# Optimization experiments

Hardware: AMD Instinct MI355X
Metric: run time of the kernel (lower is better)

Reference implementation:

```python
import jax, jax.numpy as jnp
import numpy as np

B, N, C, K, H = 64, 4096, 256, 8, 256  # H = max(dim, hidden_dim=128)
ITERS = 3
EPS = 1e-8


def _ln(x, g, b):
    # torch LayerNorm: biased variance, eps=1e-5
    m = x.mean(-1, keepdims=True)
    v = ((x - m) ** 2).mean(-1, keepdims=True)
    return (x - m) * jax.lax.rsqrt(v + 1e-5) * g + b


def setup_inputs() -> dict:
    key = jax.random.key(0)
    ks = jax.random.split(key, 16)
    s = 0.02
    d = {}
    d['inputs'] = jax.random.normal(ks[0], (B, N, C), jnp.float32)
    d['slots_noise'] = jax.random.normal(ks[1], (K, C), jnp.float32)  # eval-mode shared noise
    d['mu'] = jax.random.normal(ks[2], (C,), jnp.float32)
    d['log_sigma'] = jax.random.normal(ks[3], (C,), jnp.float32) * 0.1
    d['ln_in_g'] = jnp.ones((C,), jnp.float32); d['ln_in_b'] = jnp.zeros((C,), jnp.float32)
    d['ln_s_g'] = jnp.ones((C,), jnp.float32); d['ln_s_b'] = jnp.zeros((C,), jnp.float32)
    d['ln_ff_g'] = jnp.ones((C,), jnp.float32); d['ln_ff_b'] = jnp.zeros((C,), jnp.float32)
    d['Wq'] = jax.random.normal(ks[4], (C, C), jnp.float32) * s; d['bq'] = jnp.zeros((C,), jnp.float32)
    d['Wk'] = jax.random.normal(ks[5], (C, C), jnp.float32) * s; d['bk'] = jnp.zeros((C,), jnp.float32)
    d['Wv'] = jax.random.normal(ks[6], (C, C), jnp.float32) * s; d['bv'] = jnp.zeros((C,), jnp.float32)
    d['W_ih'] = jax.random.normal(ks[7], (C, 3 * C), jnp.float32) * s; d['b_ih'] = jnp.zeros((3 * C,), jnp.float32)
    d['W_hh'] = jax.random.normal(ks[8], (C, 3 * C), jnp.float32) * s; d['b_hh'] = jnp.zeros((3 * C,), jnp.float32)
    d['W1'] = jax.random.normal(ks[9], (C, H), jnp.float32) * s; d['b1'] = jnp.zeros((H,), jnp.float32)
    d['W2'] = jax.random.normal(ks[10], (H, C), jnp.float32) * s; d['b2'] = jnp.zeros((C,), jnp.float32)
    return d


def reference(inputs, slots_noise, mu, log_sigma,
              ln_in_g, ln_in_b, ln_s_g, ln_s_b, ln_ff_g, ln_ff_b,
              Wq, bq, Wk, bk, Wv, bv,
              W_ih, b_ih, W_hh, b_hh,
              W1, b1, W2, b2):
    scale = C ** (-0.5)
    # eval-mode slot init: mu + exp(log_sigma) * noise, shared across batch
    slots = jnp.broadcast_to(mu + jnp.exp(log_sigma) * slots_noise, (B, K, C))
    x = _ln(inputs, ln_in_g, ln_in_b)
    k = x @ Wk + bk  # [B,N,C]
    v = x @ Wv + bv  # [B,N,C]
    for _ in range(ITERS):
        slots_prev = slots
        sn = _ln(slots, ln_s_g, ln_s_b)
        q = sn @ Wq + bq  # [B,K,C]
        dots = jnp.einsum('bid,bjd->bij', q, k) * scale  # [B,K,N]
        attn = jax.nn.softmax(dots, axis=1) + EPS  # softmax over slots (queries)
        attn = attn / attn.sum(-1, keepdims=True)  # renormalize over keys
        updates = jnp.einsum('bjd,bij->bid', v, attn)  # [B,K,C]
        # torch GRUCell
        gx = updates @ W_ih + b_ih
        gh = slots_prev @ W_hh + b_hh
        xr, xz, xn = jnp.split(gx, 3, axis=-1)
        hr, hz, hn = jnp.split(gh, 3, axis=-1)
        r = jax.nn.sigmoid(xr + hr)
        z = jax.nn.sigmoid(xz + hz)
        n = jnp.tanh(xn + r * hn)
        slots = (1.0 - z) * n + z * slots_prev
        pre = _ln(slots, ln_ff_g, ln_ff_b)
        slots = slots + (jax.nn.relu(pre @ W1 + b1) @ W2 + b2)
    return slots
```

## Files before the change

kernel.cpp:

```cpp
#include <hip/hip_runtime.h>
#include <hip/hip_bf16.h>

#define B_ 64
#define N_ 4096
#define C_ 256
#define K_ 8
#define M_ (B_*N_)
#define ITERS_ 3
#define SCALE_ 0.0625f
#define EPS_ 1e-8f

typedef __attribute__((ext_vector_type(4))) float f32x4;
typedef __attribute__((ext_vector_type(8))) __bf16 bf16x8;
typedef __attribute__((ext_vector_type(8))) unsigned short ushort8;
typedef __attribute__((ext_vector_type(4))) unsigned short ushort4v;

static __device__ __forceinline__ unsigned short f2bf(float f){
    union { float f; unsigned u; } v; v.f = f;
    unsigned r = v.u + 0x7fffu + ((v.u >> 16) & 1u);
    return (unsigned short)(r >> 16);
}
static __device__ __forceinline__ float bf2f(unsigned short h){
    union { unsigned u; float f; } v; v.u = ((unsigned)h) << 16;
    return v.f;
}

__global__ void prep1_kernel(const float* __restrict__ mu, const float* __restrict__ lsig,
                             const float* __restrict__ noise, float* __restrict__ slots){
    int idx = blockIdx.x*256 + threadIdx.x;
    int c = idx & 255, i = (idx >> 8) & 7;
    slots[idx] = mu[c] + expf(lsig[c])*noise[i*256 + c];
}

__global__ void prep2_kernel(const float* __restrict__ Wq, const float* __restrict__ Wk,
                             const float* __restrict__ bq, const float* __restrict__ bk,
                             float* __restrict__ WqkT, float* __restrict__ bqt,
                             float* __restrict__ wqb, float* __restrict__ bqkv){
    __shared__ float wqrow[256], bkl[256], bql[256];
    __shared__ float red[4], red2[4];
    const int t = threadIdx.x, c = blockIdx.x;
    wqrow[t] = Wq[(size_t)c*256 + t];
    bkl[t] = bk[t];
    bql[t] = bq[t];
    __syncthreads();
    float acc = 0.f, accb = 0.f;
    const float* wkr = Wk + (size_t)t*256;
    #pragma unroll 4
    for (int d = 0; d < 256; d += 4){
        float4 wk4 = *(const float4*)(wkr + d);
        float4 wq4 = *(const float4*)(&wqrow[d]);
        float4 bq4 = *(const float4*)(&bql[d]);
        acc  += wq4.x*wk4.x + wq4.y*wk4.y + wq4.z*wk4.z + wq4.w*wk4.w;
        accb += bq4.x*wk4.x + bq4.y*wk4.y + bq4.z*wk4.z + bq4.w*wk4.w;
    }
    WqkT[(size_t)c*256 + t] = acc;
    if (c == 0) bqt[t] = accb;
    float pw = wqrow[t]*bkl[t];
    float pb = bql[t]*bkl[t];
    #pragma unroll
    for (int m = 1; m < 64; m <<= 1){ pw += __shfl_xor(pw, m); pb += __shfl_xor(pb, m); }
    if ((t & 63) == 0){ red[t >> 6] = pw; red2[t >> 6] = pb; }
    __syncthreads();
    if (t == 0){
        wqb[c] = red[0] + red[1] + red[2] + red[3];
        if (c == 0) bqkv[0] = red2[0] + red2[1] + red2[2] + red2[3];
    }
}

__global__ void ln_kernel(const float* __restrict__ x, const float* __restrict__ g,
                          const float* __restrict__ bta, unsigned short* __restrict__ XH){
    const int t = threadIdx.x;
    const int row = blockIdx.x*32 + (t >> 3), s = t & 7;
    const float* xr = x + (size_t)row*C_;
    float v[32];
    #pragma unroll
    for (int q = 0; q < 8; ++q)
        *(float4*)&v[q*4] = *(const float4*)(xr + s*4 + q*32);
    float sum = 0.f, sq = 0.f;
    #pragma unroll
    for (int e = 0; e < 32; ++e){ sum += v[e]; sq += v[e]*v[e]; }
    #pragma unroll
    for (int m = 1; m < 8; m <<= 1){ sum += __shfl_xor(sum, m); sq += __shfl_xor(sq, m); }
    float mean = sum * (1.f/256.f);
    float rstd = rsqrtf(sq * (1.f/256.f) - mean*mean + 1e-5f);
    const int jt = row >> 8, rloc = row & 255;
    #pragma unroll
    for (int q = 0; q < 8; ++q){
        float4 g4 = *(const float4*)(g + q*32 + s*4);
        float4 b4 = *(const float4*)(bta + q*32 + s*4);
        ushort4v pk;
        pk[0] = f2bf((v[q*4+0] - mean)*rstd*g4.x + b4.x);
        pk[1] = f2bf((v[q*4+1] - mean)*rstd*g4.y + b4.y);
        pk[2] = f2bf((v[q*4+2] - mean)*rstd*g4.z + b4.z);
        pk[3] = f2bf((v[q*4+3] - mean)*rstd*g4.w + b4.w);
        *(ushort4v*)(XH + (((size_t)jt*8 + q)*256 + rloc)*32 + s*4) = pk;
    }
}

__global__ void slotq_kernel(const float* __restrict__ slots, const float* __restrict__ WqkT,
                             const float* __restrict__ bqt, const float* __restrict__ wqb,
                             const float* __restrict__ bqkv, const float* __restrict__ gs,
                             const float* __restrict__ bs, float* __restrict__ qtbuf,
                             float* __restrict__ qbb){
    __shared__ float sn[8][260];
    const int t = threadIdx.x, b = blockIdx.x, cgb = blockIdx.y;
    const int i = t >> 6, l = t & 63;
    {
        float4 v4 = *(const float4*)(slots + ((size_t)b*8 + i)*256 + l*4);
        float sum = v4.x + v4.y + v4.z + v4.w;
        float sq  = v4.x*v4.x + v4.y*v4.y + v4.z*v4.z + v4.w*v4.w;
        #pragma unroll
        for (int m = 1; m < 64; m <<= 1){ sum += __shfl_xor(sum, m); sq += __shfl_xor(sq, m); }
        float mean = sum * (1.f/256.f);
        float rstd = rsqrtf(sq * (1.f/256.f) - mean*mean + 1e-5f);
        float4 g4 = *(const float4*)(gs + l*4);
        float4 b4 = *(const float4*)(bs + l*4);
        float n0 = (v4.x - mean)*rstd*g4.x + b4.x;
        float n1 = (v4.y - mean)*rstd*g4.y + b4.y;
        float n2 = (v4.z - mean)*rstd*g4.z + b4.z;
        float n3 = (v4.w - mean)*rstd*g4.w + b4.w;
        sn[i][l*4+0] = n0; sn[i][l*4+1] = n1; sn[i][l*4+2] = n2; sn[i][l*4+3] = n3;
        if (cgb == 0){
            float4 w4 = *(const float4*)(wqb + l*4);
            float pb = n0*w4.x + n1*w4.y + n2*w4.z + n3*w4.w;
            #pragma unroll
            for (int m = 1; m < 64; m <<= 1) pb += __shfl_xor(pb, m);
            if (l == 0) qbb[(size_t)b*8 + i] = SCALE_*(pb + bqkv[0]);
        }
    }
    __syncthreads();
    const int col = cgb*64 + l;
    float acc = bqt[col];
    #pragma unroll
    for (int cb = 0; cb < 256; cb += 64){
        float w[64];
        #pragma unroll
        for (int u = 0; u < 64; ++u) w[u] = WqkT[(size_t)(cb+u)*256 + col];
        #pragma unroll
        for (int u = 0; u < 64; ++u) acc += sn[i][cb+u]*w[u];
    }
    qtbuf[((size_t)b*8 + i)*256 + col] = SCALE_*acc;
}

__global__ __launch_bounds__(512)
void attn_kernel(const unsigned short* __restrict__ XH, const float* __restrict__ qt,
                 const float* __restrict__ qb, float* __restrict__ Spart,
                 float* __restrict__ Upart){
    __shared__ __align__(16) unsigned short xs[2*16384];
    __shared__ __align__(16) unsigned short pst[16*72];
    __shared__ float swred[4][8];
    const int t = threadIdx.x, b = blockIdx.x, jb = blockIdx.y;
    const unsigned short* XB = XH + (size_t)(b*16 + jb)*65536;
    const int wv = t >> 6, l = t & 63;
    const int bi = l & 15, kg = l >> 4;
    const bool isQK = (wv < 4), isPV = (wv >= 4);

    bf16x8 bfrag[8];
    float qbl = 0.f;
    {
        const ushort8 zz = (ushort8){0,0,0,0,0,0,0,0};
        #pragma unroll
        for (int ks = 0; ks < 8; ++ks) bfrag[ks] = __builtin_bit_cast(bf16x8, zz);
        if (isQK && bi < 8){
            #pragma unroll
            for (int ks = 0; ks < 8; ++ks){
                const float* qp = qt + ((size_t)b*8 + bi)*256 + ks*32 + kg*8;
                float4 qa = *(const float4*)qp;
                float4 qc = *(const float4*)(qp + 4);
                ushort8 pk;
                pk[0]=f2bf(qa.x); pk[1]=f2bf(qa.y); pk[2]=f2bf(qa.z); pk[3]=f2bf(qa.w);
                pk[4]=f2bf(qc.x); pk[5]=f2bf(qc.y); pk[6]=f2bf(qc.z); pk[7]=f2bf(qc.w);
                bfrag[ks] = __builtin_bit_cast(bf16x8, pk);
            }
            qbl = qb[(size_t)b*8 + bi];
        }
    }
    ushort8 SbA[4], SbB[4];
    const int strow[4] = { (l >> 2), 16 + (l >> 2), 32 + (l >> 2), 48 + (l >> 2) };
    f32x4 acc[4];
    #pragma unroll
    for (int n = 0; n < 4; ++n) acc[n] = (f32x4){0.f,0.f,0.f,0.f};
    const int pv_lo = bi & 7;
    const int pv_sl = (bi >> 3) ^ (kg << 1);
    float s8loc = 0.f;

#define STG_LOAD(Sb, ch) { \
    const unsigned short* gp = XB + (size_t)wv*8192 + (ch)*2048 + l*8; \
    _Pragma("unroll") for (int u = 0; u < 4; ++u) Sb[u] = *(const ushort8*)(gp + u*512); }
#define STG_WRITE(Sb, ch) { \
    unsigned short* xw = &xs[((ch)&1)*16384]; \
    _Pragma("unroll") for (int u = 0; u < 4; ++u){ \
        int rr = strow[u]; \
        int o = (wv*4 + (l & 3)) ^ ((rr & 7) ^ (((rr >> 3) & 3) << 1)); \
        *(ushort8*)&xw[rr*256 + o*8] = Sb[u]; } }
#define BARR() { asm volatile("s_waitcnt lgkmcnt(0)" ::: "memory"); __builtin_amdgcn_s_barrier(); }

#define QK_PHASE(p) if (isQK){ \
    const int cur = ((p)&1)*16384; \
    f32x4 qacc = (f32x4){0.f,0.f,0.f,0.f}; \
    const int rowL = wv*16 + bi; \
    const int swrow = (rowL & 7) ^ (((rowL >> 3) & 3) << 1); \
    const unsigned short* xrow = &xs[cur + rowL*256]; \
    _Pragma("unroll") for (int ks = 0; ks < 8; ++ks){ \
        int chn = (ks*4 + kg) ^ swrow; \
        bf16x8 af = *(const bf16x8*)&xrow[chn*8]; \
        qacc = __builtin_amdgcn_mfma_f32_16x16x32_bf16(af, bfrag[ks], qacc, 0, 0, 0); } \
    ushort4v p4; \
    _Pragma("unroll") for (int rr = 0; rr < 4; ++rr){ \
        float d = qacc[rr] + qbl; \
        float mx = d; \
        mx = fmaxf(mx, __shfl_xor(mx, 1)); \
        mx = fmaxf(mx, __shfl_xor(mx, 2)); \
        mx = fmaxf(mx, __shfl_xor(mx, 4)); \
        float e = __expf(d - mx); \
        float se = e; \
        se += __shfl_xor(se, 1); \
        se += __shfl_xor(se, 2); \
        se += __shfl_xor(se, 4); \
        float pv = e/se + EPS_; \
        p4[rr] = f2bf(pv); \
        if (bi < 8) s8loc += pv; } \
    if (bi < 8) *(ushort4v*)&pst[bi*72 + wv*16 + kg*4] = p4; }

#define PV_PHASE(p) if (isPV){ \
    const int cur = ((p)&1)*16384; \
    _Pragma("unroll") for (int kh = 0; kh < 2; ++kh){ \
        ushort8 pa = *(const ushort8*)&pst[bi*72 + kh*32 + kg*8]; \
        _Pragma("unroll") for (int n = 0; n < 4; ++n){ \
            const int ct2 = ((wv - 4)*4 + n) << 1; \
            ushort8 xv; \
            _Pragma("unroll") for (int e = 0; e < 8; ++e){ \
                int slot = ct2 ^ pv_sl ^ e; \
                xv[e] = xs[cur + kh*8192 + kg*2048 + e*256 + (slot << 3) + pv_lo]; } \
            acc[n] = __builtin_amdgcn_mfma_f32_16x16x32_bf16( \
                __builtin_bit_cast(bf16x8, pa), __builtin_bit_cast(bf16x8, xv), acc[n], 0, 0, 0); } } }

    STG_LOAD(SbA, 0); STG_WRITE(SbA, 0);
    STG_LOAD(SbB, 1);
    BARR();

    STG_LOAD(SbA, 2);
    QK_PHASE(0)
    BARR();
    PV_PHASE(0)
    STG_WRITE(SbB, 1);
    BARR();
    STG_LOAD(SbB, 3);
    QK_PHASE(1)
    BARR();
    PV_PHASE(1)
    STG_WRITE(SbA, 2);
    BARR();
    QK_PHASE(2)
    BARR();
    PV_PHASE(2)
    STG_WRITE(SbB, 3);
    BARR();
    QK_PHASE(3)
    BARR();
    PV_PHASE(3)

    if (isQK){
        float s = s8loc;
        s += __shfl_xor(s, 16);
        s += __shfl_xor(s, 32);
        if (l < 8) swred[wv][l] = s;
    }
    BARR();
    if (t < 8)
        Spart[((size_t)(b*16 + jb))*8 + t] =
            swred[0][t] + swred[1][t] + swred[2][t] + swred[3][t];
    if (isPV && kg < 2){
        #pragma unroll
        for (int n = 0; n < 4; ++n){
            const int ct = (wv - 4)*4 + n;
            #pragma unroll
            for (int r2 = 0; r2 < 4; ++r2){
                int i = kg*4 + r2;
                Upart[(((size_t)(b*16 + jb))*8 + i)*256 + ct*16 + bi] = acc[n][r2];
            }
        }
    }
#undef STG_LOAD
#undef STG_WRITE
#undef BARR
#undef QK_PHASE
#undef PV_PHASE
}

__global__ void slotu1_kernel(const float* __restrict__ slots, const float* __restrict__ Spart,
                              const float* __restrict__ Upart, const float* __restrict__ Wv,
                              const float* __restrict__ bv, const float* __restrict__ W_ih,
                              const float* __restrict__ b_ih, const float* __restrict__ W_hh,
                              const float* __restrict__ b_hh, float* __restrict__ slots2){
    __shared__ float us[8][260], sp[8][260], upd[8][260];
    const int t = threadIdx.x, b = blockIdx.x, ng = blockIdx.y;
    const int i = t >> 6, l = t & 63;
    {
        float a0 = 0.f, a1 = 0.f, a2 = 0.f, a3 = 0.f, S = 0.f;
        #pragma unroll
        for (int jbl = 0; jbl < 16; ++jbl){
            float4 u4 = *(const float4*)(Upart + (((size_t)(b*16 + jbl))*8 + i)*256 + l*4);
            a0 += u4.x; a1 += u4.y; a2 += u4.z; a3 += u4.w;
            S += Spart[((size_t)(b*16 + jbl))*8 + i];
        }
        float invS = 1.f / S;
        us[i][l*4+0] = a0*invS; us[i][l*4+1] = a1*invS;
        us[i][l*4+2] = a2*invS; us[i][l*4+3] = a3*invS;
        float4 s4 = *(const float4*)(slots + ((size_t)b*8 + i)*256 + l*4);
        sp[i][l*4+0] = s4.x; sp[i][l*4+1] = s4.y; sp[i][l*4+2] = s4.z; sp[i][l*4+3] = s4.w;
    }
    __syncthreads();
    {
        const int c4 = l*4;
        float4 acc = *(const float4*)(bv + c4);
        #pragma unroll
        for (int cb = 0; cb < 256; cb += 16){
            float4 w4[16];
            #pragma unroll
            for (int u = 0; u < 16; ++u)
                w4[u] = *(const float4*)(Wv + (size_t)(cb+u)*256 + c4);
            #pragma unroll
            for (int u = 0; u < 16; ++u){
                float uv = us[i][cb+u];
                acc.x += uv*w4[u].x; acc.y += uv*w4[u].y;
                acc.z += uv*w4[u].z; acc.w += uv*w4[u].w;
            }
        }
        *(float4*)&upd[i][c4] = acc;
    }
    __syncthreads();
    {
        const int n = ng*64 + l;
        float xr = b_ih[n], xz = b_ih[256+n], xn = b_ih[512+n];
        float hr = b_hh[n], hz = b_hh[256+n], hn = b_hh[512+n];
        #pragma unroll 2
        for (int cb = 0; cb < 256; cb += 8){
            float wi0[8], wi1[8], wi2[8], wh0[8], wh1[8], wh2[8];
            #pragma unroll
            for (int u = 0; u < 8; ++u){
                const float* wi = W_ih + (size_t)(cb+u)*768 + n;
                const float* wh = W_hh + (size_t)(cb+u)*768 + n;
                wi0[u] = wi[0]; wi1[u] = wi[256]; wi2[u] = wi[512];
                wh0[u] = wh[0]; wh1[u] = wh[256]; wh2[u] = wh[512];
            }
            #pragma unroll
            for (int u = 0; u < 8; ++u){
                float uv = upd[i][cb+u], sv = sp[i][cb+u];
                xr += uv*wi0[u]; xz += uv*wi1[u]; xn += uv*wi2[u];
                hr += sv*wh0[u]; hz += sv*wh1[u]; hn += sv*wh2[u];
            }
        }
        float rv = 1.f/(1.f + __expf(-(xr + hr)));
        float zv = 1.f/(1.f + __expf(-(xz + hz)));
        float nn = tanhf(xn + rv*hn);
        slots2[((size_t)b*8 + i)*256 + n] = (1.f - zv)*nn + zv*sp[i][n];
    }
}

__global__ void slotu2_kernel(const float* __restrict__ slots2, const float* __restrict__ gf,
                              const float* __restrict__ bf, const float* __restrict__ W1,
                              const float* __restrict__ b1, const float* __restrict__ W2,
                              const float* __restrict__ b2, float* __restrict__ slots,
                              float* __restrict__ dout){
    __shared__ float s0[8][260], pre[8][260], hb[8][260];
    const int t = threadIdx.x, b = blockIdx.x, ng = blockIdx.y;
    const int i = t >> 6, l = t & 63;
    {
        float4 v4 = *(const float4*)(slots2 + ((size_t)b*8 + i)*256 + l*4);
        float sum = v4.x + v4.y + v4.z + v4.w;
        float sq  = v4.x*v4.x + v4.y*v4.y + v4.z*v4.z + v4.w*v4.w;
        #pragma unroll
        for (int m = 1; m < 64; m <<= 1){ sum += __shfl_xor(sum, m); sq += __shfl_xor(sq, m); }
        float mean = sum * (1.f/256.f);
        float rstd = rsqrtf(sq * (1.f/256.f) - mean*mean + 1e-5f);
        float4 g4 = *(const float4*)(gf + l*4);
        float4 b4 = *(const float4*)(bf + l*4);
        s0[i][l*4+0] = v4.x; s0[i][l*4+1] = v4.y; s0[i][l*4+2] = v4.z; s0[i][l*4+3] = v4.w;
        pre[i][l*4+0] = (v4.x - mean)*rstd*g4.x + b4.x;
        pre[i][l*4+1] = (v4.y - mean)*rstd*g4.y + b4.y;
        pre[i][l*4+2] = (v4.z - mean)*rstd*g4.z + b4.z;
        pre[i][l*4+3] = (v4.w - mean)*rstd*g4.w + b4.w;
    }
    __syncthreads();
    {
        const int h4 = l*4;
        float4 acc = *(const float4*)(b1 + h4);
        #pragma unroll
        for (int cb = 0; cb < 256; cb += 16){
            float4 w4[16];
            #pragma unroll
            for (int u = 0; u < 16; ++u)
                w4[u] = *(const float4*)(W1 + (size_t)(cb+u)*256 + h4);
            #pragma unroll
            for (int u = 0; u < 16; ++u){
                float pv = pre[i][cb+u];
                acc.x += pv*w4[u].x; acc.y += pv*w4[u].y;
                acc.z += pv*w4[u].z; acc.w += pv*w4[u].w;
            }
        }
        hb[i][h4+0] = fmaxf(acc.x, 0.f); hb[i][h4+1] = fmaxf(acc.y, 0.f);
        hb[i][h4+2] = fmaxf(acc.z, 0.f); hb[i][h4+3] = fmaxf(acc.w, 0.f);
    }
    __syncthreads();
    {
        const int n = ng*64 + l;
        float acc = b2[n];
        #pragma unroll
        for (int mb = 0; mb < 256; mb += 64){
            float w[64];
            #pragma unroll
            for (int u = 0; u < 64; ++u) w[u] = W2[(size_t)(mb+u)*256 + n];
            #pragma unroll
            for (int u = 0; u < 64; ++u) acc += hb[i][mb+u]*w[u];
        }
        float val = s0[i][n] + acc;
        size_t off = ((size_t)b*8 + i)*256 + n;
        slots[off] = val;
        dout[off]  = val;
    }
}

extern "C" void kernel_launch(void* const* d_in, const int* in_sizes, int n_in,
                              void* d_out, int out_size, void* d_ws, size_t ws_size,
                              hipStream_t stream){
    const float* inputs = (const float*)d_in[0];
    const float* noise  = (const float*)d_in[1];
    const float* mu     = (const float*)d_in[2];
    const float* lsig   = (const float*)d_in[3];
    const float* g_in   = (const float*)d_in[4];
    const float* b_in   = (const float*)d_in[5];
    const float* g_s    = (const float*)d_in[6];
    const float* b_s    = (const float*)d_in[7];
    const float* g_ff   = (const float*)d_in[8];
    const float* b_ff   = (const float*)d_in[9];
    const float* Wq     = (const float*)d_in[10];
    const float* bq     = (const float*)d_in[11];
    const float* Wk     = (const float*)d_in[12];
    const float* bk     = (const float*)d_in[13];
    const float* Wv     = (const float*)d_in[14];
    const float* bv     = (const float*)d_in[15];
    const float* W_ih   = (const float*)d_in[16];
    const float* b_ih   = (const float*)d_in[17];
    const float* W_hh   = (const float*)d_in[18];
    const float* b_hh   = (const float*)d_in[19];
    const float* W1     = (const float*)d_in[20];
    const float* b1     = (const float*)d_in[21];
    const float* W2     = (const float*)d_in[22];
    const float* b2     = (const float*)d_in[23];

    char* ws = (char*)d_ws;
    unsigned short* XH  = (unsigned short*)(ws);
    float* Upart        = (float*)(ws + ((size_t)128 << 20));
    float* Spart        = (float*)(ws + ((size_t)136 << 20));
    float* qtbuf        = (float*)(ws + ((size_t)137 << 20));
    float* qbb          = (float*)(ws + ((size_t)138 << 20));
    float* slots        = (float*)(ws + ((size_t)139 << 20));
    float* slots2       = (float*)(ws + ((size_t)140 << 20));
    float* WqkT         = (float*)(ws + ((size_t)141 << 20));
    float* bqt          = (float*)(ws + ((size_t)142 << 20));
    float* wqb          = (float*)(ws + ((size_t)143 << 20));
    float* bqkv         = (float*)(ws + ((size_t)144 << 20));

    prep1_kernel<<<512, 256, 0, stream>>>(mu, lsig, noise, slots);
    prep2_kernel<<<256, 256, 0, stream>>>(Wq, Wk, bq, bk, WqkT, bqt, wqb, bqkv);
    ln_kernel<<<M_/32, 256, 0, stream>>>(inputs, g_in, b_in, XH);
    for (int it = 0; it < ITERS_; ++it){
        slotq_kernel<<<dim3(B_, 4), 512, 0, stream>>>(slots, WqkT, bqt, wqb, bqkv,
                                                      g_s, b_s, qtbuf, qbb);
        attn_kernel<<<dim3(B_, 16), 512, 0, stream>>>(XH, qtbuf, qbb, Spart, Upart);
        slotu1_kernel<<<dim3(B_, 4), 512, 0, stream>>>(slots, Spart, Upart, Wv, bv,
                                                       W_ih, b_ih, W_hh, b_hh, slots2);
        slotu2_kernel<<<dim3(B_, 4), 512, 0, stream>>>(slots2, g_ff, b_ff, W1, b1, W2, b2,
                                                       slots, (float*)d_out);
    }
}
```

Before: 473.1 us.

## Fuse per-iteration slot update and query projection into one kernel

Merges the slot-query, GRU and MLP kernels into a single per-batch kernel that runs after each attention pass. It also computes the next iteration's query there, so each iteration needs one slot kernel launch instead of three and the intermediate slots2 round trip through global memory goes away. The precomputed Wq·Wkᵀ fusion is replaced by two projections per iteration, q then q·Wkᵀ, using a transposed Wk built in the prep kernel. In exchange the slot work now runs on 64 blocks instead of 256, so each block does four times the serial weight streaming. The last launch also computes a query that is never used.

```diff
diff --git a/kernel.cpp b/kernel.cpp
--- a/kernel.cpp
+++ b/kernel.cpp
@@ -25,45 +25,15 @@
     return v.f;
 }
 
-__global__ void prep1_kernel(const float* __restrict__ mu, const float* __restrict__ lsig,
-                             const float* __restrict__ noise, float* __restrict__ slots){
+__global__ void prep_kernel(const float* __restrict__ mu, const float* __restrict__ lsig,
+                            const float* __restrict__ noise, const float* __restrict__ Wk,
+                            float* __restrict__ slots, float* __restrict__ WkT){
     int idx = blockIdx.x*256 + threadIdx.x;
     int c = idx & 255, i = (idx >> 8) & 7;
     slots[idx] = mu[c] + expf(lsig[c])*noise[i*256 + c];
-}
-
-__global__ void prep2_kernel(const float* __restrict__ Wq, const float* __restrict__ Wk,
-                             const float* __restrict__ bq, const float* __restrict__ bk,
-                             float* __restrict__ WqkT, float* __restrict__ bqt,
-                             float* __restrict__ wqb, float* __restrict__ bqkv){
-    __shared__ float wqrow[256], bkl[256], bql[256];
-    __shared__ float red[4], red2[4];
-    const int t = threadIdx.x, c = blockIdx.x;
-    wqrow[t] = Wq[(size_t)c*256 + t];
-    bkl[t] = bk[t];
-    bql[t] = bq[t];
-    __syncthreads();
-    float acc = 0.f, accb = 0.f;
-    const float* wkr = Wk + (size_t)t*256;
-    #pragma unroll 4
-    for (int d = 0; d < 256; d += 4){
-        float4 wk4 = *(const float4*)(wkr + d);
-        float4 wq4 = *(const float4*)(&wqrow[d]);
-        float4 bq4 = *(const float4*)(&bql[d]);
-        acc  += wq4.x*wk4.x + wq4.y*wk4.y + wq4.z*wk4.z + wq4.w*wk4.w;
-        accb += bq4.x*wk4.x + bq4.y*wk4.y + bq4.z*wk4.z + bq4.w*wk4.w;
-    }
-    WqkT[(size_t)c*256 + t] = acc;
-    if (c == 0) bqt[t] = accb;
-    float pw = wqrow[t]*bkl[t];
-    float pb = bql[t]*bkl[t];
-    #pragma unroll
-    for (int m = 1; m < 64; m <<= 1){ pw += __shfl_xor(pw, m); pb += __shfl_xor(pb, m); }
-    if ((t & 63) == 0){ red[t >> 6] = pw; red2[t >> 6] = pb; }
-    __syncthreads();
-    if (t == 0){
-        wqb[c] = red[0] + red[1] + red[2] + red[3];
-        if (c == 0) bqkv[0] = red2[0] + red2[1] + red2[2] + red2[3];
+    if (idx < 65536){
+        int cc = idx >> 8, d = idx & 255;
+        WkT[idx] = Wk[(size_t)d*256 + cc];
     }
 }
 
@@ -97,51 +67,6 @@
     }
 }
 
-__global__ void slotq_kernel(const float* __restrict__ slots, const float* __restrict__ WqkT,
-                             const float* __restrict__ bqt, const float* __restrict__ wqb,
-                             const float* __restrict__ bqkv, const float* __restrict__ gs,
-                             const float* __restrict__ bs, float* __restrict__ qtbuf,
-                             float* __restrict__ qbb){
-    __shared__ float sn[8][260];
-    const int t = threadIdx.x, b = blockIdx.x, cgb = blockIdx.y;
-    const int i = t >> 6, l = t & 63;
-    {
-        float4 v4 = *(const float4*)(slots + ((size_t)b*8 + i)*256 + l*4);
-        float sum = v4.x + v4.y + v4.z + v4.w;
-        float sq  = v4.x*v4.x + v4.y*v4.y + v4.z*v4.z + v4.w*v4.w;
-        #pragma unroll
-        for (int m = 1; m < 64; m <<= 1){ sum += __shfl_xor(sum, m); sq += __shfl_xor(sq, m); }
-        float mean = sum * (1.f/256.f);
-        float rstd = rsqrtf(sq * (1.f/256.f) - mean*mean + 1e-5f);
-        float4 g4 = *(const float4*)(gs + l*4);
-        float4 b4 = *(const float4*)(bs + l*4);
-        float n0 = (v4.x - mean)*rstd*g4.x + b4.x;
-        float n1 = (v4.y - mean)*rstd*g4.y + b4.y;
-        float n2 = (v4.z - mean)*rstd*g4.z + b4.z;
-        float n3 = (v4.w - mean)*rstd*g4.w + b4.w;
-        sn[i][l*4+0] = n0; sn[i][l*4+1] = n1; sn[i][l*4+2] = n2; sn[i][l*4+3] = n3;
-        if (cgb == 0){
-            float4 w4 = *(const float4*)(wqb + l*4);
-            float pb = n0*w4.x + n1*w4.y + n2*w4.z + n3*w4.w;
-            #pragma unroll
-            for (int m = 1; m < 64; m <<= 1) pb += __shfl_xor(pb, m);
-            if (l == 0) qbb[(size_t)b*8 + i] = SCALE_*(pb + bqkv[0]);
-        }
-    }
-    __syncthreads();
-    const int col = cgb*64 + l;
-    float acc = bqt[col];
-    #pragma unroll
-    for (int cb = 0; cb < 256; cb += 64){
-        float w[64];
-        #pragma unroll
-        for (int u = 0; u < 64; ++u) w[u] = WqkT[(size_t)(cb+u)*256 + col];
-        #pragma unroll
-        for (int u = 0; u < 64; ++u) acc += sn[i][cb+u]*w[u];
-    }
-    qtbuf[((size_t)b*8 + i)*256 + col] = SCALE_*acc;
-}
-
 __global__ __launch_bounds__(512)
 void attn_kernel(const unsigned short* __restrict__ XH, const float* __restrict__ qt,
                  const float* __restrict__ qb, float* __restrict__ Spart,
@@ -288,136 +213,222 @@
 #undef PV_PHASE
 }
 
-__global__ void slotu1_kernel(const float* __restrict__ slots, const float* __restrict__ Spart,
-                              const float* __restrict__ Upart, const float* __restrict__ Wv,
-                              const float* __restrict__ bv, const float* __restrict__ W_ih,
-                              const float* __restrict__ b_ih, const float* __restrict__ W_hh,
-                              const float* __restrict__ b_hh, float* __restrict__ slots2){
-    __shared__ float us[8][260], sp[8][260], upd[8][260];
-    const int t = threadIdx.x, b = blockIdx.x, ng = blockIdx.y;
-    const int i = t >> 6, l = t & 63;
+__global__ void slotU_kernel(int first, const float* __restrict__ Spart, const float* __restrict__ Upart,
+                             const float* __restrict__ Wv, const float* __restrict__ bv,
+                             const float* __restrict__ W_ih, const float* __restrict__ b_ih,
+                             const float* __restrict__ W_hh, const float* __restrict__ b_hh,
+                             const float* __restrict__ gf, const float* __restrict__ bf,
+                             const float* __restrict__ W1, const float* __restrict__ b1,
+                             const float* __restrict__ W2, const float* __restrict__ b2,
+                             const float* __restrict__ gs, const float* __restrict__ bs,
+                             const float* __restrict__ Wq, const float* __restrict__ bq,
+                             const float* __restrict__ WkT, const float* __restrict__ bk,
+                             float* __restrict__ slots, float* __restrict__ qtbuf,
+                             float* __restrict__ qbb, float* __restrict__ dout){
+    __shared__ float us[8][260], sp[8][260], upd[8][260], s2[8][260];
+    __shared__ float pre[8][260], hb[8][260], sn[8][260], qv[8][260];
+    const int t = threadIdx.x, b = blockIdx.x;
+    const int i = t >> 6, l = t & 63, c0 = l*4;
+
+    if (!first){
+        {
+            float a0=0.f, a1=0.f, a2=0.f, a3=0.f, S=0.f;
+            #pragma unroll
+            for (int jb = 0; jb < 16; ++jb){
+                float4 u4 = *(const float4*)(Upart + (((size_t)(b*16 + jb))*8 + i)*256 + c0);
+                a0 += u4.x; a1 += u4.y; a2 += u4.z; a3 += u4.w;
+                S += Spart[((size_t)(b*16 + jb))*8 + i];
+            }
+            float invS = 1.f / S;
+            us[i][c0+0] = a0*invS; us[i][c0+1] = a1*invS;
+            us[i][c0+2] = a2*invS; us[i][c0+3] = a3*invS;
+            float4 s4 = *(const float4*)(slots + ((size_t)b*8 + i)*256 + c0);
+            sp[i][c0+0] = s4.x; sp[i][c0+1] = s4.y; sp[i][c0+2] = s4.z; sp[i][c0+3] = s4.w;
+        }
+        __syncthreads();
+        {
+            float4 acc = *(const float4*)(bv + c0);
+            #pragma unroll 2
+            for (int cb = 0; cb < 256; cb += 16){
+                float4 w4[16];
+                #pragma unroll
+                for (int u = 0; u < 16; ++u)
+                    w4[u] = *(const float4*)(Wv + (size_t)(cb+u)*256 + c0);
+                #pragma unroll
+                for (int u = 0; u < 16; ++u){
+                    float uv = us[i][cb+u];
+                    acc.x += uv*w4[u].x; acc.y += uv*w4[u].y;
+                    acc.z += uv*w4[u].z; acc.w += uv*w4[u].w;
+                }
+            }
+            *(float4*)&upd[i][c0] = acc;
+        }
+        __syncthreads();
+        {
+            float4 xr = *(const float4*)(b_ih + c0);
+            float4 xz = *(const float4*)(b_ih + 256 + c0);
+            float4 xn = *(const float4*)(b_ih + 512 + c0);
+            float4 hr = *(const float4*)(b_hh + c0);
+            float4 hz = *(const float4*)(b_hh + 256 + c0);
+            float4 hn = *(const float4*)(b_hh + 512 + c0);
+            for (int cb = 0; cb < 256; cb += 4){
+                float4 wi0[4], wi1[4], wi2[4], wh0[4], wh1[4], wh2[4];
+                #pragma unroll
+                for (int u = 0; u < 4; ++u){
+                    const float* wi = W_ih + (size_t)(cb+u)*768 + c0;
+                    const float* wh = W_hh + (size_t)(cb+u)*768 + c0;
+                    wi0[u] = *(const float4*)(wi);
+                    wi1[u] = *(const float4*)(wi + 256);
+                    wi2[u] = *(const float4*)(wi + 512);
+                    wh0[u] = *(const float4*)(wh);
+                    wh1[u] = *(const float4*)(wh + 256);
+                    wh2[u] = *(const float4*)(wh + 512);
+                }
+                #pragma unroll
+                for (int u = 0; u < 4; ++u){
+                    float uv = upd[i][cb+u], sv = sp[i][cb+u];
+                    xr.x += uv*wi0[u].x; xr.y += uv*wi0[u].y; xr.z += uv*wi0[u].z; xr.w += uv*wi0[u].w;
+                    xz.x += uv*wi1[u].x; xz.y += uv*wi1[u].y; xz.z += uv*wi1[u].z; xz.w += uv*wi1[u].w;
+                    xn.x += uv*wi2[u].x; xn.y += uv*wi2[u].y; xn.z += uv*wi2[u].z; xn.w += uv*wi2[u].w;
+                    hr.x += sv*wh0[u].x; hr.y += sv*wh0[u].y; hr.z += sv*wh0[u].z; hr.w += sv*wh0[u].w;
+                    hz.x += sv*wh1[u].x; hz.y += sv*wh1[u].y; hz.z += sv*wh1[u].z; hz.w += sv*wh1[u].w;
+                    hn.x += sv*wh2[u].x; hn.y += sv*wh2[u].y; hn.z += sv*wh2[u].z; hn.w += sv*wh2[u].w;
+                }
+            }
+            #pragma unroll
+            for (int e = 0; e < 4; ++e){
+                float xre = ((const float*)&xr)[e], xze = ((const float*)&xz)[e], xne = ((const float*)&xn)[e];
+                float hre = ((const float*)&hr)[e], hze = ((const float*)&hz)[e], hne = ((const float*)&hn)[e];
+                float rv = 1.f/(1.f + __expf(-(xre + hre)));
+                float zv = 1.f/(1.f + __expf(-(xze + hze)));
+                float nn = tanhf(xne + rv*hne);
+                s2[i][c0+e] = (1.f - zv)*nn + zv*sp[i][c0+e];
+            }
+        }
+        __syncthreads();
+        {
+            float v0 = s2[i][c0+0], v1 = s2[i][c0+1], v2 = s2[i][c0+2], v3 = s2[i][c0+3];
+            float sum = v0+v1+v2+v3;
+            float sq  = v0*v0+v1*v1+v2*v2+v3*v3;
+            #pragma unroll
+            for (int m = 1; m < 64; m <<= 1){ sum += __shfl_xor(sum, m); sq += __shfl_xor(sq, m); }
+            float mean = sum * (1.f/256.f);
+            float rstd = rsqrtf(sq * (1.f/256.f) - mean*mean + 1e-5f);
+            float4 g4 = *(const float4*)(gf + c0);
+            float4 b4 = *(const float4*)(bf + c0);
+            pre[i][c0+0] = (v0 - mean)*rstd*g4.x + b4.x;
+            pre[i][c0+1] = (v1 - mean)*rstd*g4.y + b4.y;
+            pre[i][c0+2] = (v2 - mean)*rstd*g4.z + b4.z;
+            pre[i][c0+3] = (v3 - mean)*rstd*g4.w + b4.w;
+        }
+        __syncthreads();
+        {
+            float4 acc = *(const float4*)(b1 + c0);
+            #pragma unroll 2
+            for (int cb = 0; cb < 256; cb += 16){
+                float4 w4[16];
+                #pragma unroll
+                for (int u = 0; u < 16; ++u)
+                    w4[u] = *(const float4*)(W1 + (size_t)(cb+u)*256 + c0);
+                #pragma unroll
+                for (int u = 0; u < 16; ++u){
+                    float pv = pre[i][cb+u];
+                    acc.x += pv*w4[u].x; acc.y += pv*w4[u].y;
+                    acc.z += pv*w4[u].z; acc.w += pv*w4[u].w;
+                }
+            }
+            hb[i][c0+0] = fmaxf(acc.x, 0.f); hb[i][c0+1] = fmaxf(acc.y, 0.f);
+            hb[i][c0+2] = fmaxf(acc.z, 0.f); hb[i][c0+3] = fmaxf(acc.w, 0.f);
+        }
+        __syncthreads();
+        {
+            float4 acc = *(const float4*)(b2 + c0);
+            #pragma unroll 2
+            for (int mb = 0; mb < 256; mb += 16){
+                float4 w4[16];
+                #pragma unroll
+                for (int u = 0; u < 16; ++u)
+                    w4[u] = *(const float4*)(W2 + (size_t)(mb+u)*256 + c0);
+                #pragma unroll
+                for (int u = 0; u < 16; ++u){
+                    float hv = hb[i][mb+u];
+                    acc.x += hv*w4[u].x; acc.y += hv*w4[u].y;
+                    acc.z += hv*w4[u].z; acc.w += hv*w4[u].w;
+                }
+            }
+            float4 fin;
+            fin.x = s2[i][c0+0] + acc.x; fin.y = s2[i][c0+1] + acc.y;
+            fin.z = s2[i][c0+2] + acc.z; fin.w = s2[i][c0+3] + acc.w;
+            size_t off = ((size_t)b*8 + i)*256 + c0;
+            *(float4*)(slots + off) = fin;
+            *(float4*)(dout + off)  = fin;
+            sp[i][c0+0] = fin.x; sp[i][c0+1] = fin.y; sp[i][c0+2] = fin.z; sp[i][c0+3] = fin.w;
+        }
+        __syncthreads();
+    } else {
+        float4 s4 = *(const float4*)(slots + ((size_t)b*8 + i)*256 + c0);
+        sp[i][c0+0] = s4.x; sp[i][c0+1] = s4.y; sp[i][c0+2] = s4.z; sp[i][c0+3] = s4.w;
+        __syncthreads();
+    }
+
     {
-        float a0 = 0.f, a1 = 0.f, a2 = 0.f, a3 = 0.f, S = 0.f;
-        #pragma unroll
-        for (int jbl = 0; jbl < 16; ++jbl){
-            float4 u4 = *(const float4*)(Upart + (((size_t)(b*16 + jbl))*8 + i)*256 + l*4);
-            a0 += u4.x; a1 += u4.y; a2 += u4.z; a3 += u4.w;
-            S += Spart[((size_t)(b*16 + jbl))*8 + i];
-        }
-        float invS = 1.f / S;
-        us[i][l*4+0] = a0*invS; us[i][l*4+1] = a1*invS;
-        us[i][l*4+2] = a2*invS; us[i][l*4+3] = a3*invS;
-        float4 s4 = *(const float4*)(slots + ((size_t)b*8 + i)*256 + l*4);
-        sp[i][l*4+0] = s4.x; sp[i][l*4+1] = s4.y; sp[i][l*4+2] = s4.z; sp[i][l*4+3] = s4.w;
-    }
-    __syncthreads();
-    {
-        const int c4 = l*4;
-        float4 acc = *(const float4*)(bv + c4);
-        #pragma unroll
-        for (int cb = 0; cb < 256; cb += 16){
-            float4 w4[16];
-            #pragma unroll
-            for (int u = 0; u < 16; ++u)
-                w4[u] = *(const float4*)(Wv + (size_t)(cb+u)*256 + c4);
-            #pragma unroll
-            for (int u = 0; u < 16; ++u){
-                float uv = us[i][cb+u];
-                acc.x += uv*w4[u].x; acc.y += uv*w4[u].y;
-                acc.z += uv*w4[u].z; acc.w += uv*w4[u].w;
-            }
-        }
-        *(float4*)&upd[i][c4] = acc;
-    }
-    __syncthreads();
-    {
-        const int n = ng*64 + l;
-        float xr = b_ih[n], xz = b_ih[256+n], xn = b_ih[512+n];
-        float hr = b_hh[n], hz = b_hh[256+n], hn = b_hh[512+n];
-        #pragma unroll 2
-        for (int cb = 0; cb < 256; cb += 8){
-            float wi0[8], wi1[8], wi2[8], wh0[8], wh1[8], wh2[8];
-            #pragma unroll
-            for (int u = 0; u < 8; ++u){
-                const float* wi = W_ih + (size_t)(cb+u)*768 + n;
-                const float* wh = W_hh + (size_t)(cb+u)*768 + n;
-                wi0[u] = wi[0]; wi1[u] = wi[256]; wi2[u] = wi[512];
-                wh0[u] = wh[0]; wh1[u] = wh[256]; wh2[u] = wh[512];
-            }
-            #pragma unroll
-            for (int u = 0; u < 8; ++u){
-                float uv = upd[i][cb+u], sv = sp[i][cb+u];
-                xr += uv*wi0[u]; xz += uv*wi1[u]; xn += uv*wi2[u];
-                hr += sv*wh0[u]; hz += sv*wh1[u]; hn += sv*wh2[u];
-            }
-        }
-        float rv = 1.f/(1.f + __expf(-(xr + hr)));
-        float zv = 1.f/(1.f + __expf(-(xz + hz)));
-        float nn = tanhf(xn + rv*hn);
-        slots2[((size_t)b*8 + i)*256 + n] = (1.f - zv)*nn + zv*sp[i][n];
-    }
-}
-
-__global__ void slotu2_kernel(const float* __restrict__ slots2, const float* __restrict__ gf,
-                              const float* __restrict__ bf, const float* __restrict__ W1,
-                              const float* __restrict__ b1, const float* __restrict__ W2,
-                              const float* __restrict__ b2, float* __restrict__ slots,
-                              float* __restrict__ dout){
-    __shared__ float s0[8][260], pre[8][260], hb[8][260];
-    const int t = threadIdx.x, b = blockIdx.x, ng = blockIdx.y;
-    const int i = t >> 6, l = t & 63;
-    {
-        float4 v4 = *(const float4*)(slots2 + ((size_t)b*8 + i)*256 + l*4);
-        float sum = v4.x + v4.y + v4.z + v4.w;
-        float sq  = v4.x*v4.x + v4.y*v4.y + v4.z*v4.z + v4.w*v4.w;
+        float v0 = sp[i][c0+0], v1 = sp[i][c0+1], v2 = sp[i][c0+2], v3 = sp[i][c0+3];
+        float sum = v0+v1+v2+v3;
+        float sq  = v0*v0+v1*v1+v2*v2+v3*v3;
         #pragma unroll
         for (int m = 1; m < 64; m <<= 1){ sum += __shfl_xor(sum, m); sq += __shfl_xor(sq, m); }
         float mean = sum * (1.f/256.f);
         float rstd = rsqrtf(sq * (1.f/256.f) - mean*mean + 1e-5f);
-        float4 g4 = *(const float4*)(gf + l*4);
-        float4 b4 = *(const float4*)(bf + l*4);
-        s0[i][l*4+0] = v4.x; s0[i][l*4+1] = v4.y; s0[i][l*4+2] = v4.z; s0[i][l*4+3] = v4.w;
-        pre[i][l*4+0] = (v4.x - mean)*rstd*g4.x + b4.x;
-        pre[i][l*4+1] = (v4.y - mean)*rstd*g4.y + b4.y;
-        pre[i][l*4+2] = (v4.z - mean)*rstd*g4.z + b4.z;
-        pre[i][l*4+3] = (v4.w - mean)*rstd*g4.w + b4.w;
+        float4 g4 = *(const float4*)(gs + c0);
+        float4 b4 = *(const float4*)(bs + c0);
+        sn[i][c0+0] = (v0 - mean)*rstd*g4.x + b4.x;
+        sn[i][c0+1] = (v1 - mean)*rstd*g4.y + b4.y;
+        sn[i][c0+2] = (v2 - mean)*rstd*g4.z + b4.z;
+        sn[i][c0+3] = (v3 - mean)*rstd*g4.w + b4.w;
     }
     __syncthreads();
     {
-        const int h4 = l*4;
-        float4 acc = *(const float4*)(b1 + h4);
-        #pragma unroll
+        float4 acc = *(const float4*)(bq + c0);
+        #pragma unroll 2
         for (int cb = 0; cb < 256; cb += 16){
             float4 w4[16];
             #pragma unroll
             for (int u = 0; u < 16; ++u)
-                w4[u] = *(const float4*)(W1 + (size_t)(cb+u)*256 + h4);
+                w4[u] = *(const float4*)(Wq + (size_t)(cb+u)*256 + c0);
             #pragma unroll
             for (int u = 0; u < 16; ++u){
-                float pv = pre[i][cb+u];
-                acc.x += pv*w4[u].x; acc.y += pv*w4[u].y;
-                acc.z += pv*w4[u].z; acc.w += pv*w4[u].w;
-            }
-        }
-        hb[i][h4+0] = fmaxf(acc.x, 0.f); hb[i][h4+1] = fmaxf(acc.y, 0.f);
-        hb[i][h4+2] = fmaxf(acc.z, 0.f); hb[i][h4+3] = fmaxf(acc.w, 0.f);
+                float sv = sn[i][cb+u];
+                acc.x += sv*w4[u].x; acc.y += sv*w4[u].y;
+                acc.z += sv*w4[u].z; acc.w += sv*w4[u].w;
+            }
+        }
+        qv[i][c0+0] = acc.x; qv[i][c0+1] = acc.y;
+        qv[i][c0+2] = acc.z; qv[i][c0+3] = acc.w;
     }
     __syncthreads();
     {
-        const int n = ng*64 + l;
-        float acc = b2[n];
+        float4 acc = (float4){0.f,0.f,0.f,0.f};
+        #pragma unroll 2
+        for (int cb = 0; cb < 256; cb += 16){
+            float4 w4[16];
+            #pragma unroll
+            for (int u = 0; u < 16; ++u)
+                w4[u] = *(const float4*)(WkT + (size_t)(cb+u)*256 + c0);
+            #pragma unroll
+            for (int u = 0; u < 16; ++u){
+                float qvv = qv[i][cb+u];
+                acc.x += qvv*w4[u].x; acc.y += qvv*w4[u].y;
+                acc.z += qvv*w4[u].z; acc.w += qvv*w4[u].w;
+            }
+        }
+        float4 o;
+        o.x = SCALE_*acc.x; o.y = SCALE_*acc.y; o.z = SCALE_*acc.z; o.w = SCALE_*acc.w;
+        *(float4*)(qtbuf + ((size_t)b*8 + i)*256 + c0) = o;
+        float4 k4 = *(const float4*)(bk + c0);
+        float pb = qv[i][c0+0]*k4.x + qv[i][c0+1]*k4.y + qv[i][c0+2]*k4.z + qv[i][c0+3]*k4.w;
         #pragma unroll
-        for (int mb = 0; mb < 256; mb += 64){
-            float w[64];
-            #pragma unroll
-            for (int u = 0; u < 64; ++u) w[u] = W2[(size_t)(mb+u)*256 + n];
-            #pragma unroll
-            for (int u = 0; u < 64; ++u) acc += hb[i][mb+u]*w[u];
-        }
-        float val = s0[i][n] + acc;
-        size_t off = ((size_t)b*8 + i)*256 + n;
-        slots[off] = val;
-        dout[off]  = val;
+        for (int m = 1; m < 64; m <<= 1) pb += __shfl_xor(pb, m);
+        if (l == 0) qbb[(size_t)b*8 + i] = SCALE_*pb;
     }
 }
 
@@ -456,22 +467,17 @@
     float* qtbuf        = (float*)(ws + ((size_t)137 << 20));
     float* qbb          = (float*)(ws + ((size_t)138 << 20));
     float* slots        = (float*)(ws + ((size_t)139 << 20));
-    float* slots2       = (float*)(ws + ((size_t)140 << 20));
-    float* WqkT         = (float*)(ws + ((size_t)141 << 20));
-    float* bqt          = (float*)(ws + ((size_t)142 << 20));
-    float* wqb          = (float*)(ws + ((size_t)143 << 20));
-    float* bqkv         = (float*)(ws + ((size_t)144 << 20));
-
-    prep1_kernel<<<512, 256, 0, stream>>>(mu, lsig, noise, slots);
-    prep2_kernel<<<256, 256, 0, stream>>>(Wq, Wk, bq, bk, WqkT, bqt, wqb, bqkv);
+    float* WkT          = (float*)(ws + ((size_t)140 << 20));
+
+    prep_kernel<<<512, 256, 0, stream>>>(mu, lsig, noise, Wk, slots, WkT);
+    slotU_kernel<<<B_, 512, 0, stream>>>(1, Spart, Upart, Wv, bv, W_ih, b_ih, W_hh, b_hh,
+                                         g_ff, b_ff, W1, b1, W2, b2, g_s, b_s, Wq, bq,
+                                         WkT, bk, slots, qtbuf, qbb, (float*)d_out);
     ln_kernel<<<M_/32, 256, 0, stream>>>(inputs, g_in, b_in, XH);
     for (int it = 0; it < ITERS_; ++it){
-        slotq_kernel<<<dim3(B_, 4), 512, 0, stream>>>(slots, WqkT, bqt, wqb, bqkv,
-                                                      g_s, b_s, qtbuf, qbb);
         attn_kernel<<<dim3(B_, 16), 512, 0, stream>>>(XH, qtbuf, qbb, Spart, Upart);
-        slotu1_kernel<<<dim3(B_, 4), 512, 0, stream>>>(slots, Spart, Upart, Wv, bv,
-                                                       W_ih, b_ih, W_hh, b_hh, slots2);
-        slotu2_kernel<<<dim3(B_, 4), 512, 0, stream>>>(slots2, g_ff, b_ff, W1, b1, W2, b2,
-                                                       slots, (float*)d_out);
-    }
-}
+        slotU_kernel<<<B_, 512, 0, stream>>>(0, Spart, Upart, Wv, bv, W_ih, b_ih, W_hh, b_hh,
+                                             g_ff, b_ff, W1, b1, W2, b2, g_s, b_s, Wq, bq,
+                                             WkT, bk, slots, qtbuf, qbb, (float*)d_out);
+    }
+}
```

Result: slower. 800.1 us (+69.1%).
